# Performance work log

Measured on AMD Instinct MI355X. Metric: run time of the kernel, lower is better.

## Reference

```python
import jax, jax.numpy as jnp
import numpy as np

B, N, E = 64, 2048, 32768          # graphs, nodes/graph, edges/graph
DIM = 64
RATIO = 0.8
K1 = int(np.ceil(RATIO * N))        # 1639 nodes/graph after pool1
K2 = int(np.ceil(RATIO * K1))       # 1312 nodes/graph after pool2
NUM_CLASSES = 6


def gcn_conv(x, W, b, src, dst, valid, n):
    # GCNConv with self-loops: out = D^-1/2 (A+I) D^-1/2 (x W) + b
    xw = x @ W                                          # [n, DIM]
    deg = jnp.zeros(n, x.dtype).at[dst].add(valid) + 1.0  # in-degree incl. self-loop
    norm = valid * jax.lax.rsqrt(deg[src] * deg[dst])      # per-edge norm (0 for masked)
    agg = jnp.zeros_like(xw).at[dst].add(xw[src] * norm[:, None])
    return agg + xw / deg[:, None] + b                  # self-loop term has norm 1/deg


def topk_pool(x, p, n_graphs, n_per, k):
    # PyG TopKPooling: score = tanh(x.p/||p||); keep top-k per graph; gate x by score
    score = jnp.tanh((x @ p) / jnp.linalg.norm(p))       # [n_graphs*n_per]
    vals, idx = jax.lax.top_k(score.reshape(n_graphs, n_per), k)  # [n_graphs, k]
    xg = x.reshape(n_graphs, n_per, -1)
    sel = jnp.take_along_axis(xg, idx[..., None], axis=1)          # [n_graphs, k, DIM]
    xp = sel * vals[..., None]
    perm = (idx + (jnp.arange(n_graphs) * n_per)[:, None]).reshape(-1)  # global ids kept
    return xp.reshape(n_graphs * k, -1), perm


def global_max_mean(x, n_graphs, n_per):
    xg = x.reshape(n_graphs, n_per, -1)
    return jnp.concatenate([xg.max(axis=1), xg.mean(axis=1)], axis=1)  # [n_graphs, 2*DIM]


def forward(x, edge_index, batch, W1, b1, p1, W2, b2, p2, lin1_w, lin1_b, lin2_w, lin2_b):
    src, dst = edge_index[0], edge_index[1]
    n_total = B * N
    ones = jnp.ones(src.shape[0], x.dtype)

    x = jax.nn.relu(gcn_conv(x, W1, b1, src, dst, ones, n_total))
    x, perm = topk_pool(x, p1, B, N, K1)
    x1 = global_max_mean(x, B, K1)

    # filter_adj: reindex edges to surviving nodes; drop (mask) edges touching removed nodes
    new_id = jnp.full(n_total, -1, jnp.int32).at[perm].set(jnp.arange(B * K1, dtype=jnp.int32))
    s2, d2 = new_id[src], new_id[dst]
    valid = ((s2 >= 0) & (d2 >= 0)).astype(x.dtype)
    s2 = jnp.where(s2 >= 0, s2, 0)
    d2 = jnp.where(d2 >= 0, d2, 0)

    x = jax.nn.relu(gcn_conv(x, W2, b2, s2, d2, valid, B * K1))
    x, _ = topk_pool(x, p2, B, K1, K2)
    x2 = global_max_mean(x, B, K2)

    h = x1 + x2
    h = jax.nn.relu(h @ lin1_w + lin1_b)
    return h @ lin2_w + lin2_b                           # [B, NUM_CLASSES]


def setup_inputs():
    key = jax.random.key(0)
    ks = jax.random.split(key, 10)
    x = jax.random.normal(ks[0], (B * N, DIM), jnp.float32)
    off = (jnp.arange(B) * N)[:, None]
    src = (jax.random.randint(ks[1], (B, E), 0, N) + off).reshape(-1)
    dst = (jax.random.randint(ks[2], (B, E), 0, N) + off).reshape(-1)
    edge_index = jnp.stack([src, dst]).astype(jnp.int32)
    batch = jnp.repeat(jnp.arange(B, dtype=jnp.int32), N)
    s = 1.0 / np.sqrt(DIM)
    return {
        "x": x,
        "edge_index": edge_index,
        "batch": batch,
        "W1": jax.random.normal(ks[3], (DIM, DIM), jnp.float32) * s,
        "b1": jnp.zeros(DIM, jnp.float32),
        "p1": jax.random.normal(ks[4], (DIM,), jnp.float32) * s,
        "W2": jax.random.normal(ks[5], (DIM, DIM), jnp.float32) * s,
        "b2": jnp.zeros(DIM, jnp.float32),
        "p2": jax.random.normal(ks[6], (DIM,), jnp.float32) * s,
        "lin1_w": jax.random.normal(ks[7], (2 * DIM, DIM), jnp.float32) / np.sqrt(2 * DIM),
        "lin1_b": jnp.zeros(DIM, jnp.float32),
        "lin2_w": jax.random.normal(ks[8], (DIM, NUM_CLASSES), jnp.float32) * s,
        "lin2_b": jnp.zeros(NUM_CLASSES, jnp.float32),
    }


def reference(x, edge_index, batch, W1, b1, p1, W2, b2, p2, lin1_w, lin1_b, lin2_w, lin2_b):
    return forward(x, edge_index, batch, W1, b1, p1, W2, b2, p2, lin1_w, lin1_b, lin2_w, lin2_b)
```

## Files before the change

kernel.cpp:

```cpp
#include <hip/hip_runtime.h>
#include <hip/hip_bf16.h>
#include <cstdint>
#include <cstddef>

#define B_    64
#define N_    2048
#define E_    32768
#define DIM_  64
#define K1_   1639
#define K2_   1312
#define NTOT  (B_ * N_)
#define ETOT  (B_ * E_)
#define N2TOT (B_ * K1_)
#define NCLS  6
#define PB_   8
#define CHUNKS_ 16
#define SLICES_ 16
#define BCAP  3072
#define REG_  192

typedef short bf8 __attribute__((ext_vector_type(8)));
typedef float f4  __attribute__((ext_vector_type(4)));

static __device__ __forceinline__ float2 bf2f(unsigned u) {
    float2 r;
    r.x = __uint_as_float(u << 16);
    r.y = __uint_as_float(u & 0xFFFF0000u);
    return r;
}
static __device__ __forceinline__ unsigned f2bf(float a, float b) {
    __hip_bfloat162 h = __float22bfloat162_rn(make_float2(a, b));
    unsigned u;
    __builtin_memcpy(&u, &h, 4);
    return u;
}
static __device__ __forceinline__ unsigned short f2bf_rn(float v) {
    unsigned u = __float_as_uint(v);
    return (unsigned short)((u + 0x7FFFu + ((u >> 16) & 1u)) >> 16);
}
static __device__ __forceinline__ unsigned long long mk_key(float s, int i) {
    unsigned u = __float_as_uint(s);
    u = (u & 0x80000000u) ? ~u : (u | 0x80000000u);
    return ((unsigned long long)u << 11) | (unsigned long long)(2047 - i);
}

template<int STAGE>
__launch_bounds__(256)
__global__ void k_bucket(const int* src, const int* dst, const int* remap,
                         int* bcnt, unsigned int* blist) {
    const int LSTR = (STAGE == 1) ? 128 : 103;
    __shared__ unsigned int lb[CHUNKS_][REG_];
    __shared__ int lc[CHUNKS_];
    __shared__ int rm[N_];
    int b = blockIdx.x;
    int g = b & 63, slice = b >> 6;
    int tid = threadIdx.x;
    if (tid < CHUNKS_) lc[tid] = 0;
    if (STAGE == 2)
        for (int i = tid; i < N_; i += 256) rm[i] = remap[g * N_ + i];
    __syncthreads();
    const int ESL = E_ / SLICES_;
    const int* sp = src + (size_t)g * E_ + slice * ESL;
    const int* dp = dst + (size_t)g * E_ + slice * ESL;
    int gbase = g * ((STAGE == 1) ? N_ : K1_);
    for (int e = tid * 4; e < ESL; e += 1024) {
        int4 ss = *(const int4*)&sp[e];
        int4 dd = *(const int4*)&dp[e];
#pragma unroll
        for (int t = 0; t < 4; t++) {
            int s = (&ss.x)[t], d = (&dd.x)[t];
            if (STAGE == 2) {
                s = rm[s & (N_ - 1)]; d = rm[d & (N_ - 1)];
                if ((s | d) < 0) continue;
                s -= gbase; d -= gbase;
            } else {
                s &= (N_ - 1); d &= (N_ - 1);
            }
            int ch = d / LSTR;
            int dl = d - ch * LSTR;
            int p = atomicAdd(&lc[ch], 1);
            if (p < REG_) lb[ch][p] = ((unsigned)dl << 12) | (unsigned)s;
        }
    }
    __syncthreads();
    for (int ch = 0; ch < CHUNKS_; ch++) {
        int n = min(lc[ch], REG_);
        unsigned int* out = blist + (size_t)(g * CHUNKS_ + ch) * BCAP + slice * REG_;
        for (int i = tid; i < n; i += 256) out[i] = lb[ch][i];
    }
    if (tid < CHUNKS_) bcnt[(g * SLICES_ + slice) * CHUNKS_ + tid] = min(lc[tid], REG_);
}

template<int STAGE>
__launch_bounds__(256)
__global__ void k_sort(const int* bcnt, unsigned int* blist,
                       const float* xf, const unsigned int* xg,
                       unsigned int* xb, int* ninfo) {
    const int NL   = (STAGE == 1) ? N_ : K1_;
    const int LSTR = (STAGE == 1) ? 128 : 103;
    __shared__ int cnt[128], st[128], cur[128], cnt_s[SLICES_], stot[2];
    __shared__ float rsqv[128];
    __shared__ unsigned short sorted[BCAP];
    int b = blockIdx.x;
    int g = b & 63, ch = b >> 6;
    int tid = threadIdx.x;
    if (tid < 128) { cnt[tid] = 0; cur[tid] = 0; }
    if (tid < SLICES_) cnt_s[tid] = bcnt[(g * SLICES_ + tid) * CHUNKS_ + ch];
    __syncthreads();
    size_t bb = (size_t)(g * CHUNKS_ + ch) * BCAP;
    const unsigned int* bl = blist + bb;
    const int TOT = SLICES_ * REG_;
    for (int i = tid; i < TOT; i += 256) {
        int s = i / REG_, j = i - s * REG_;
        if (j < cnt_s[s]) atomicAdd(&cnt[bl[i] >> 12], 1);
    }
    __syncthreads();
    if (tid < 128) {
        int v = cnt[tid];
        int l64 = tid & 63;
#pragma unroll
        for (int o = 1; o < 64; o <<= 1) {
            int t = __shfl_up(v, o);
            if (l64 >= o) v += t;
        }
        st[tid] = v;
        if (l64 == 63) stot[tid >> 6] = v;
    }
    __syncthreads();
    if (tid >= 64 && tid < 128) st[tid] += stot[0];
    __syncthreads();
    for (int i = tid; i < TOT; i += 256) {
        int s = i / REG_, j = i - s * REG_;
        if (j < cnt_s[s]) {
            unsigned pk = bl[i];
            int dl = (int)(pk >> 12);
            int p = st[dl] - cnt[dl] + atomicAdd(&cur[dl], 1);
            sorted[p] = (unsigned short)(pk & 0xFFFu);
        }
    }
    __syncthreads();
    int n = st[127];
    for (int i = tid; i < n; i += 256) blist[bb + i] = ((unsigned int)sorted[i]) << 5;
    int lo = ch * LSTR;
    int nloc = min(LSTR, NL - lo);
    int gbase = g * NL;
    if (tid < nloc) {
        int node = gbase + lo + tid;
        int c = cnt[tid];
        int start = (int)bb + st[tid] - c;
        ninfo[node] = (start << 8) | min(c, 255);
        rsqv[tid] = rsqrtf((float)(c + 1));
    }
    __syncthreads();
    for (int idx = tid; idx < nloc * 32; idx += 256) {
        int nl = idx >> 5, f2 = idx & 31;
        int node = gbase + lo + nl;
        float sc = rsqv[nl];
        float2 v;
        if (STAGE == 1) v = ((const float2*)xf)[(size_t)node * 32 + f2];
        else            v = bf2f(xg[(size_t)node * 32 + f2]);
        xb[(size_t)node * 32 + f2] = f2bf(v.x * sc, v.y * sc);
    }
}

template<bool GATE>
__launch_bounds__(256)
__global__ void k_agg(const unsigned int* xb, const int* ninfo, const unsigned int* csr,
                      float* y) {
    int b = blockIdx.x;
    int xcd = b & 7, r = b >> 3;
    int wid = threadIdx.x >> 6, lane = threadIdx.x & 63;
    int half = lane >> 5;
    int sub = wid * 2 + half;
    int graph, local;
    if (GATE) {
        graph = xcd * 8 + r / 205;
        local = (r % 205) * 8 + sub;
        if (local >= K1_) return;
    } else {
        graph = xcd * 8 + (r >> 8);
        local = (r & 255) * 8 + sub;
    }
    const int NL = GATE ? K1_ : N_;
    int node = graph * NL + local;
    int l32 = lane & 31;
    int hbase = half << 5;
    int ni = ninfo[node];
    int cnt = ni & 255, base = ni >> 8;
    float rd = rsqrtf((float)(cnt + 1));
    float a0x = 0.f, a0y = 0.f, a1x = 0.f, a1y = 0.f;
    float a2x = 0.f, a2y = 0.f, a3x = 0.f, a3y = 0.f;
    int gbase32 = graph * NL * 32;
    for (int chunk = 0; chunk < cnt; chunk += 32) {
        int nch = min(32, cnt - chunk);
        int sv = 0;
        if (l32 < nch) sv = gbase32 + (int)csr[base + chunk + l32];
        int i = 0;
        for (; i + 4 <= nch; i += 4) {
            int e0 = __shfl(sv, hbase + i);
            int e1 = __shfl(sv, hbase + i + 1);
            int e2 = __shfl(sv, hbase + i + 2);
            int e3 = __shfl(sv, hbase + i + 3);
            unsigned u0 = xb[(size_t)(e0 + l32)];
            unsigned u1 = xb[(size_t)(e1 + l32)];
            unsigned u2 = xb[(size_t)(e2 + l32)];
            unsigned u3 = xb[(size_t)(e3 + l32)];
            float2 f0 = bf2f(u0), f1 = bf2f(u1), f2 = bf2f(u2), f3 = bf2f(u3);
            a0x += f0.x; a0y += f0.y;
            a1x += f1.x; a1y += f1.y;
            a2x += f2.x; a2y += f2.y;
            a3x += f3.x; a3y += f3.y;
        }
        for (; i < nch; i++) {
            int e0 = __shfl(sv, hbase + i);
            float2 f0 = bf2f(xb[(size_t)(e0 + l32)]);
            a0x += f0.x; a0y += f0.y;
        }
    }
    float sx = (a0x + a1x) + (a2x + a3x);
    float sy = (a0y + a1y) + (a2y + a3y);
    float2 fs = bf2f(xb[(size_t)node * 32 + l32]);
    float2 o;
    o.x = (sx + fs.x) * rd;
    o.y = (sy + fs.y) * rd;
    ((float2*)y)[(size_t)node * 32 + l32] = o;
}

__launch_bounds__(256)
__global__ void k_convrow(float* y, const float* W, const float* bias, const float* pvec,
                          float* score, int rows) {
    int wid  = threadIdx.x >> 6;
    int lane = threadIdx.x & 63;
    int rowbase = blockIdx.x * 64 + wid * 16;
    int q = lane >> 4, c = lane & 15;
    bf8 bh[2][4], blo[2][4];
#pragma unroll
    for (int ks = 0; ks < 2; ks++)
#pragma unroll
        for (int nt = 0; nt < 4; nt++) {
            bf8 h, l;
#pragma unroll
            for (int j = 0; j < 8; j++) {
                float wv = W[(ks * 32 + q * 8 + j) * 64 + nt * 16 + c];
                unsigned short hb = f2bf_rn(wv);
                h[j] = (short)hb;
                l[j] = (short)f2bf_rn(wv - __uint_as_float((unsigned)hb << 16));
            }
            bh[ks][nt] = h; blo[ks][nt] = l;
        }
    const float* yr = y + (size_t)(rowbase + c) * DIM_ + q * 8;
    bf8 ah[2], al[2];
#pragma unroll
    for (int ks = 0; ks < 2; ks++) {
        float4 v0 = *(const float4*)(yr + ks * 32);
        float4 v1 = *(const float4*)(yr + ks * 32 + 4);
        float vv[8] = {v0.x, v0.y, v0.z, v0.w, v1.x, v1.y, v1.z, v1.w};
        bf8 h, l;
#pragma unroll
        for (int j = 0; j < 8; j++) {
            unsigned short hb = f2bf_rn(vv[j]);
            h[j] = (short)hb;
            l[j] = (short)f2bf_rn(vv[j] - __uint_as_float((unsigned)hb << 16));
        }
        ah[ks] = h; al[ks] = l;
    }
    float pp = 0.f;
#pragma unroll
    for (int i = 0; i < DIM_; i++) pp += pvec[i] * pvec[i];
    float rpn = rsqrtf(pp);
    float dot[4] = {0.f, 0.f, 0.f, 0.f};
#pragma unroll
    for (int nt = 0; nt < 4; nt++) {
        f4 acc = {0.f, 0.f, 0.f, 0.f};
#pragma unroll
        for (int ks = 0; ks < 2; ks++) {
            acc = __builtin_amdgcn_mfma_f32_16x16x32_bf16(ah[ks], bh[ks][nt],  acc, 0, 0, 0);
            acc = __builtin_amdgcn_mfma_f32_16x16x32_bf16(ah[ks], blo[ks][nt], acc, 0, 0, 0);
            acc = __builtin_amdgcn_mfma_f32_16x16x32_bf16(al[ks], bh[ks][nt],  acc, 0, 0, 0);
        }
        float bcol = bias[nt * 16 + c];
        float pcol = pvec[nt * 16 + c];
        float st[4];
#pragma unroll
        for (int reg = 0; reg < 4; reg++) {
            float v = fmaxf(acc[reg] + bcol, 0.f);
            st[reg] = v;
            dot[reg] += v * pcol;
        }
#pragma unroll
        for (int reg = 0; reg < 4; reg++)
            y[(size_t)(rowbase + q * 4 + reg) * DIM_ + nt * 16 + c] = st[reg];
    }
#pragma unroll
    for (int m = 1; m < 16; m <<= 1) {
#pragma unroll
        for (int reg = 0; reg < 4; reg++) dot[reg] += __shfl_xor(dot[reg], m);
    }
    if (c == 0) {
#pragma unroll
        for (int reg = 0; reg < 4; reg++)
            score[rowbase + q * 4 + reg] = tanhf(dot[reg] * rpn);
    }
    (void)rows;
}

template<int STAGE>
__launch_bounds__(256)
__global__ void k_thresh(const float* score, unsigned long long* thresh) {
    const int Nin = (STAGE == 1) ? N_ : K1_;
    const int K   = (STAGE == 1) ? K1_ : K2_;
    __shared__ unsigned long long keys[N_];
    __shared__ int bins[256], wsum[4];
    __shared__ unsigned long long s_prefix;
    __shared__ int s_need;
    int g = blockIdx.x, tid = threadIdx.x;
    int l64 = tid & 63, wid = tid >> 6;
    const float* sg = score + (size_t)g * Nin;
    for (int i = tid; i < Nin; i += 256) keys[i] = mk_key(sg[i], i);
    if (tid == 0) { s_need = K; s_prefix = 0ull; }
    __syncthreads();
    for (int shift = 40; shift >= 0; shift -= 8) {
        bins[tid] = 0;
        __syncthreads();
        unsigned long long pref = s_prefix;
        int need = s_need;
        int hi = shift + 8;
        for (int i = tid; i < Nin; i += 256) {
            unsigned long long k = keys[i];
            if ((k >> hi) == pref) atomicAdd(&bins[(int)((k >> shift) & 255)], 1);
        }
        __syncthreads();
        int mine = bins[tid];
        int v = mine;
#pragma unroll
        for (int o = 1; o < 64; o <<= 1) {
            int t = __shfl_down(v, o);
            if (l64 + o < 64) v += t;
        }
        if (l64 == 0) wsum[wid] = v;
        __syncthreads();
        for (int w = wid + 1; w < 4; w++) v += wsum[w];
        int nxt = v - mine;
        if (v >= need && nxt < need) {
            s_prefix = (pref << 8) | (unsigned long long)tid;
            s_need = need - nxt;
        }
        __syncthreads();
    }
    if (tid == 0) thresh[g] = s_prefix;
}

template<int STAGE>
__launch_bounds__(256)
__global__ void k_pool(const float* score, const float* conv, const unsigned long long* thresh,
                       int* new_id, unsigned int* xg, float* part) {
    const int Nin = (STAGE == 1) ? N_ : K1_;
    const int RNG = (STAGE == 1) ? (N_ / PB_) : ((K1_ + PB_ - 1) / PB_);
    __shared__ int rnk[256];
    __shared__ unsigned char keepf[256];
    __shared__ int wsum[4], s_base[4];
    __shared__ float rmx[4][64], rsm[4][64];
    int b = blockIdx.x;
    int g = b & 63, pb = b >> 6;
    int tid = threadIdx.x;
    int l64 = tid & 63, wid = tid >> 6;
    const float* sg = score + (size_t)g * Nin;
    unsigned long long T = thresh[g];
    int R0 = pb * RNG;
    int R1 = min(R0 + RNG, Nin);
    if (STAGE == 1) {
        int cb = 0;
        for (int i = tid; i < R0; i += 256) cb += (mk_key(sg[i], i) >= T) ? 1 : 0;
#pragma unroll
        for (int o = 32; o; o >>= 1) cb += __shfl_down(cb, o);
        if (l64 == 0) s_base[wid] = cb;
        int i = R0 + tid;
        int keep = (i < R1 && mk_key(sg[i], i) >= T) ? 1 : 0;
        keepf[tid] = (unsigned char)keep;
        int v = keep;
#pragma unroll
        for (int o = 1; o < 64; o <<= 1) {
            int t = __shfl_up(v, o);
            if (l64 >= o) v += t;
        }
        if (l64 == 63) wsum[wid] = v;
        __syncthreads();
        int base = s_base[0] + s_base[1] + s_base[2] + s_base[3];
        int wbase = 0;
        for (int w = 0; w < wid; w++) wbase += wsum[w];
        int r = base + wbase + v - keep;
        rnk[tid] = r;
        if (i < Nin) new_id[g * N_ + i] = keep ? (g * K1_ + r) : -1;
    } else {
        int i = R0 + tid;
        keepf[tid] = (unsigned char)((i < R1 && mk_key(sg[i], i) >= T) ? 1 : 0);
    }
    __syncthreads();
    float mx = -3.402823466e38f, sm = 0.f;
    for (int i = R0 + wid; i < R1; i += 4) {
        if (!keepf[i - R0]) continue;
        float val = sg[i];
        float v = conv[(size_t)(g * Nin + i) * DIM_ + l64] * val;
        mx = fmaxf(mx, v);
        sm += v;
        if (STAGE == 1) {
            unsigned pk = f2bf(v, __shfl_xor(v, 1));
            if (!(l64 & 1)) xg[(size_t)(g * K1_ + rnk[i - R0]) * 32 + (l64 >> 1)] = pk;
        }
    }
    rmx[wid][l64] = mx; rsm[wid][l64] = sm;
    __syncthreads();
    if (wid == 0) {
        mx = fmaxf(fmaxf(rmx[0][l64], rmx[1][l64]), fmaxf(rmx[2][l64], rmx[3][l64]));
        sm = rsm[0][l64] + rsm[1][l64] + rsm[2][l64] + rsm[3][l64];
        part[((size_t)(g * PB_ + pb) * 2 + 0) * 64 + l64] = mx;
        part[((size_t)(g * PB_ + pb) * 2 + 1) * 64 + l64] = sm;
    }
}

__launch_bounds__(64)
__global__ void k_head(const float* part1, const float* part2,
                       const float* l1w, const float* l1b,
                       const float* l2w, const float* l2b, float* out) {
    __shared__ float h[128];
    __shared__ float h1[64];
    int g = blockIdx.x, t = threadIdx.x;
    float mx1 = -3.402823466e38f, sm1 = 0.f, mx2 = -3.402823466e38f, sm2 = 0.f;
#pragma unroll
    for (int c = 0; c < PB_; c++) {
        mx1 = fmaxf(mx1, part1[((size_t)(g * PB_ + c) * 2 + 0) * 64 + t]);
        sm1 += part1[((size_t)(g * PB_ + c) * 2 + 1) * 64 + t];
        mx2 = fmaxf(mx2, part2[((size_t)(g * PB_ + c) * 2 + 0) * 64 + t]);
        sm2 += part2[((size_t)(g * PB_ + c) * 2 + 1) * 64 + t];
    }
    h[t]      = mx1 + mx2;
    h[t + 64] = sm1 / (float)K1_ + sm2 / (float)K2_;
    __syncthreads();
    float acc = l1b[t];
#pragma unroll 8
    for (int i = 0; i < 128; i++) acc += h[i] * l1w[i * 64 + t];
    h1[t] = fmaxf(acc, 0.0f);
    __syncthreads();
    if (t < NCLS) {
        float o = l2b[t];
#pragma unroll
        for (int i = 0; i < 64; i++) o += h1[i] * l2w[i * NCLS + t];
        out[g * NCLS + t] = o;
    }
}

extern "C" void kernel_launch(void* const* d_in, const int* in_sizes, int n_in,
                              void* d_out, int out_size, void* d_ws, size_t ws_size,
                              hipStream_t stream) {
    const float* x   = (const float*)d_in[0];
    const int*   ei  = (const int*)d_in[1];
    const int*   src = ei;
    const int*   dst = ei + ETOT;
    const float* W1  = (const float*)d_in[3];
    const float* b1  = (const float*)d_in[4];
    const float* p1  = (const float*)d_in[5];
    const float* W2  = (const float*)d_in[6];
    const float* b2  = (const float*)d_in[7];
    const float* p2  = (const float*)d_in[8];
    const float* l1w = (const float*)d_in[9];
    const float* l1b = (const float*)d_in[10];
    const float* l2w = (const float*)d_in[11];
    const float* l2b = (const float*)d_in[12];
    (void)in_sizes; (void)n_in; (void)out_size; (void)ws_size;

    char* ws = (char*)d_ws;
    size_t off = 0;
    auto alloc = [&](size_t bytes) -> void* {
        void* p = ws + off;
        off = (off + bytes + 255) & ~(size_t)255;
        return p;
    };
    float*              bufA   = (float*)             alloc((size_t)NTOT  * DIM_ * 4);
    float*              bufB   = (float*)             alloc((size_t)N2TOT * DIM_ * 4);
    unsigned int*       blist  = (unsigned int*)      alloc((size_t)B_ * CHUNKS_ * BCAP * 4);
    unsigned int*       xb     = (unsigned int*)      alloc((size_t)NTOT * 32 * 4);
    int*                bcnt   = (int*)               alloc((size_t)B_ * SLICES_ * CHUNKS_ * 4);
    int*                ninfo  = (int*)               alloc((size_t)NTOT * 4);
    float*              score  = (float*)             alloc((size_t)NTOT * 4);
    int*                newid  = (int*)               alloc((size_t)NTOT * 4);
    unsigned long long* thr    = (unsigned long long*)alloc((size_t)B_ * 8);
    float*              part1  = (float*)             alloc((size_t)B_ * PB_ * 128 * 4);
    float*              part2  = (float*)             alloc((size_t)B_ * PB_ * 128 * 4);
    unsigned int*       xg     = (unsigned int*)bufB;

    k_bucket<1><<<B_ * SLICES_, 256, 0, stream>>>(src, dst, nullptr, bcnt, blist);
    k_sort<1><<<B_ * CHUNKS_, 256, 0, stream>>>(bcnt, blist, x, nullptr, xb, ninfo);
    k_agg<false><<<NTOT / 8, 256, 0, stream>>>(xb, ninfo, blist, bufA);
    k_convrow<<<NTOT / 64, 256, 0, stream>>>(bufA, W1, b1, p1, score, NTOT);
    k_thresh<1><<<B_, 256, 0, stream>>>(score, thr);
    k_pool<1><<<B_ * PB_, 256, 0, stream>>>(score, bufA, thr, newid, xg, part1);

    k_bucket<2><<<B_ * SLICES_, 256, 0, stream>>>(src, dst, newid, bcnt, blist);
    k_sort<2><<<B_ * CHUNKS_, 256, 0, stream>>>(bcnt, blist, nullptr, xg, xb, ninfo);
    k_agg<true><<<205 * B_, 256, 0, stream>>>(xb, ninfo, blist, bufB);
    k_convrow<<<N2TOT / 64, 256, 0, stream>>>(bufB, W2, b2, p2, score, N2TOT);
    k_thresh<2><<<B_, 256, 0, stream>>>(score, thr);
    k_pool<2><<<B_ * PB_, 256, 0, stream>>>(score, bufB, thr, nullptr, nullptr, part2);

    k_head<<<B_, 64, 0, stream>>>(part1, part2, l1w, l1b, l2w, l2b, (float*)d_out);
}
```

Before: 320.3 us.

## Fuse neighbor aggregation with GCN linear transform via LDS staging

Merges the gather-aggregate kernel and the MFMA row-transform kernel into one kernel per stage. Each block aggregates 64 rows into a swizzled LDS tile and feeds the MFMA transform straight from LDS, so the fp32 intermediate no longer round-trips through global memory and one launch per stage disappears. It also prefetches the next node's CSR indices and unrolls the gather loop by 8 for more loads in flight. In exchange, each block now runs far more sequential work (8 nodes per half-wave), which cuts the number of blocks and may hide gather latency less well.

```diff
diff --git a/kernel.cpp b/kernel.cpp
--- a/kernel.cpp
+++ b/kernel.cpp
@@ -165,73 +165,116 @@
 
 template<bool GATE>
 __launch_bounds__(256)
-__global__ void k_agg(const unsigned int* xb, const int* ninfo, const unsigned int* csr,
-                      float* y) {
+__global__ void k_aggconv(const unsigned int* xb, const int* ninfo, const unsigned int* csr,
+                          const float* W, const float* bias, const float* pvec,
+                          float* y, float* score) {
+    const int NL = GATE ? K1_ : N_;
+    __shared__ float4 ls4[1024];
+    float* ls = (float*)ls4;
     int b = blockIdx.x;
-    int xcd = b & 7, r = b >> 3;
+    int wg;
+    if (GATE) {
+        int xcd = b & 7, k = b >> 3;
+        wg = (xcd < 7 ? xcd * 205 : 1435 + (xcd - 7) * 204) + k;
+    } else {
+        wg = (b & 7) * 256 + (b >> 3);
+    }
     int wid = threadIdx.x >> 6, lane = threadIdx.x & 63;
     int half = lane >> 5;
-    int sub = wid * 2 + half;
-    int graph, local;
-    if (GATE) {
-        graph = xcd * 8 + r / 205;
-        local = (r % 205) * 8 + sub;
-        if (local >= K1_) return;
-    } else {
-        graph = xcd * 8 + (r >> 8);
-        local = (r & 255) * 8 + sub;
-    }
-    const int NL = GATE ? K1_ : N_;
-    int node = graph * NL + local;
     int l32 = lane & 31;
     int hbase = half << 5;
-    int ni = ninfo[node];
-    int cnt = ni & 255, base = ni >> 8;
-    float rd = rsqrtf((float)(cnt + 1));
-    float a0x = 0.f, a0y = 0.f, a1x = 0.f, a1y = 0.f;
-    float a2x = 0.f, a2y = 0.f, a3x = 0.f, a3y = 0.f;
-    int gbase32 = graph * NL * 32;
-    for (int chunk = 0; chunk < cnt; chunk += 32) {
-        int nch = min(32, cnt - chunk);
-        int sv = 0;
-        if (l32 < nch) sv = gbase32 + (int)csr[base + chunk + l32];
-        int i = 0;
-        for (; i + 4 <= nch; i += 4) {
-            int e0 = __shfl(sv, hbase + i);
-            int e1 = __shfl(sv, hbase + i + 1);
-            int e2 = __shfl(sv, hbase + i + 2);
-            int e3 = __shfl(sv, hbase + i + 3);
-            unsigned u0 = xb[(size_t)(e0 + l32)];
-            unsigned u1 = xb[(size_t)(e1 + l32)];
-            unsigned u2 = xb[(size_t)(e2 + l32)];
-            unsigned u3 = xb[(size_t)(e3 + l32)];
-            float2 f0 = bf2f(u0), f1 = bf2f(u1), f2 = bf2f(u2), f3 = bf2f(u3);
-            a0x += f0.x; a0y += f0.y;
-            a1x += f1.x; a1y += f1.y;
-            a2x += f2.x; a2y += f2.y;
-            a3x += f3.x; a3y += f3.y;
-        }
-        for (; i < nch; i++) {
-            int e0 = __shfl(sv, hbase + i);
-            float2 f0 = bf2f(xb[(size_t)(e0 + l32)]);
-            a0x += f0.x; a0y += f0.y;
-        }
-    }
-    float sx = (a0x + a1x) + (a2x + a3x);
-    float sy = (a0y + a1y) + (a2y + a3y);
-    float2 fs = bf2f(xb[(size_t)node * 32 + l32]);
-    float2 o;
-    o.x = (sx + fs.x) * rd;
-    o.y = (sy + fs.y) * rd;
-    ((float2*)y)[(size_t)node * 32 + l32] = o;
-}
-
-__launch_bounds__(256)
-__global__ void k_convrow(float* y, const float* W, const float* bias, const float* pvec,
-                          float* score, int rows) {
-    int wid  = threadIdx.x >> 6;
-    int lane = threadIdx.x & 63;
-    int rowbase = blockIdx.x * 64 + wid * 16;
+    int rowbase = wg * 64 + wid * 16;
+
+    int niv = 0;
+    if (lane < 16) niv = ninfo[rowbase + lane];
+    int ni = __shfl(niv, half);
+    int sv = 0;
+    {
+        int c0 = ni & 255;
+        if (l32 < c0) sv = (int)csr[(ni >> 8) + l32];
+    }
+#pragma unroll 1
+    for (int p = 0; p < 8; p++) {
+        int cnt = ni & 255, base = ni >> 8;
+        int ni_n = 0, sv_n = 0;
+        if (p < 7) {
+            ni_n = __shfl(niv, 2 * (p + 1) + half);
+            int cn = ni_n & 255;
+            if (l32 < cn) sv_n = (int)csr[(ni_n >> 8) + l32];
+        }
+        int rloc = wid * 16 + 2 * p + half;
+        int node = wg * 64 + rloc;
+        int gbase32 = GATE ? (node / K1_) * (K1_ * 32) : ((node & ~(N_ - 1)) * 32);
+        unsigned selfu = xb[(size_t)node * 32 + l32];
+        float a0x = 0.f, a0y = 0.f, a1x = 0.f, a1y = 0.f;
+        float a2x = 0.f, a2y = 0.f, a3x = 0.f, a3y = 0.f;
+        int svc = sv;
+        for (int chunk = 0; chunk < cnt; chunk += 32) {
+            int nch = min(32, cnt - chunk);
+            if (chunk) svc = (l32 < nch) ? (int)csr[base + chunk + l32] : 0;
+            int i = 0;
+            for (; i + 8 <= nch; i += 8) {
+                int e0 = __shfl(svc, hbase + i);
+                int e1 = __shfl(svc, hbase + i + 1);
+                int e2 = __shfl(svc, hbase + i + 2);
+                int e3 = __shfl(svc, hbase + i + 3);
+                int e4 = __shfl(svc, hbase + i + 4);
+                int e5 = __shfl(svc, hbase + i + 5);
+                int e6 = __shfl(svc, hbase + i + 6);
+                int e7 = __shfl(svc, hbase + i + 7);
+                unsigned u0 = xb[(size_t)(gbase32 + e0 + l32)];
+                unsigned u1 = xb[(size_t)(gbase32 + e1 + l32)];
+                unsigned u2 = xb[(size_t)(gbase32 + e2 + l32)];
+                unsigned u3 = xb[(size_t)(gbase32 + e3 + l32)];
+                unsigned u4 = xb[(size_t)(gbase32 + e4 + l32)];
+                unsigned u5 = xb[(size_t)(gbase32 + e5 + l32)];
+                unsigned u6 = xb[(size_t)(gbase32 + e6 + l32)];
+                unsigned u7 = xb[(size_t)(gbase32 + e7 + l32)];
+                float2 f0 = bf2f(u0), f1 = bf2f(u1), f2 = bf2f(u2), f3 = bf2f(u3);
+                float2 f4 = bf2f(u4), f5 = bf2f(u5), f6 = bf2f(u6), f7 = bf2f(u7);
+                a0x += f0.x; a0y += f0.y;
+                a1x += f1.x; a1y += f1.y;
+                a2x += f2.x; a2y += f2.y;
+                a3x += f3.x; a3y += f3.y;
+                a0x += f4.x; a0y += f4.y;
+                a1x += f5.x; a1y += f5.y;
+                a2x += f6.x; a2y += f6.y;
+                a3x += f7.x; a3y += f7.y;
+            }
+            for (; i + 4 <= nch; i += 4) {
+                int e0 = __shfl(svc, hbase + i);
+                int e1 = __shfl(svc, hbase + i + 1);
+                int e2 = __shfl(svc, hbase + i + 2);
+                int e3 = __shfl(svc, hbase + i + 3);
+                unsigned u0 = xb[(size_t)(gbase32 + e0 + l32)];
+                unsigned u1 = xb[(size_t)(gbase32 + e1 + l32)];
+                unsigned u2 = xb[(size_t)(gbase32 + e2 + l32)];
+                unsigned u3 = xb[(size_t)(gbase32 + e3 + l32)];
+                float2 f0 = bf2f(u0), f1 = bf2f(u1), f2 = bf2f(u2), f3 = bf2f(u3);
+                a0x += f0.x; a0y += f0.y;
+                a1x += f1.x; a1y += f1.y;
+                a2x += f2.x; a2y += f2.y;
+                a3x += f3.x; a3y += f3.y;
+            }
+            for (; i < nch; i++) {
+                int e0 = __shfl(svc, hbase + i);
+                float2 f0 = bf2f(xb[(size_t)(gbase32 + e0 + l32)]);
+                a0x += f0.x; a0y += f0.y;
+            }
+        }
+        float rd = rsqrtf((float)(cnt + 1));
+        float sx = (a0x + a1x) + (a2x + a3x);
+        float sy = (a0y + a1y) + (a2y + a3y);
+        float2 fs = bf2f(selfu);
+        float2 o;
+        o.x = (sx + fs.x) * rd;
+        o.y = (sy + fs.y) * rd;
+        int pi = rloc * 32 + ((((l32 >> 1) ^ (rloc & 7)) << 1) | (l32 & 1));
+        ((float2*)ls)[pi] = o;
+        ni = ni_n; sv = sv_n;
+    }
+    __syncthreads();
+
     int q = lane >> 4, c = lane & 15;
     bf8 bh[2][4], blo[2][4];
 #pragma unroll
@@ -248,12 +291,13 @@
             }
             bh[ks][nt] = h; blo[ks][nt] = l;
         }
-    const float* yr = y + (size_t)(rowbase + c) * DIM_ + q * 8;
+    int rl16 = (wid * 16 + c) * 16;
+    int cx = c & 7;
     bf8 ah[2], al[2];
 #pragma unroll
     for (int ks = 0; ks < 2; ks++) {
-        float4 v0 = *(const float4*)(yr + ks * 32);
-        float4 v1 = *(const float4*)(yr + ks * 32 + 4);
+        float4 v0 = ls4[rl16 + ((ks * 8 + q * 2 + 0) ^ cx)];
+        float4 v1 = ls4[rl16 + ((ks * 8 + q * 2 + 1) ^ cx)];
         float vv[8] = {v0.x, v0.y, v0.z, v0.w, v1.x, v1.y, v1.z, v1.w};
         bf8 h, l;
 #pragma unroll
@@ -289,7 +333,7 @@
         }
 #pragma unroll
         for (int reg = 0; reg < 4; reg++)
-            y[(size_t)(rowbase + q * 4 + reg) * DIM_ + nt * 16 + c] = st[reg];
+            y[(size_t)(wg * 64 + wid * 16 + q * 4 + reg) * DIM_ + nt * 16 + c] = st[reg];
     }
 #pragma unroll
     for (int m = 1; m < 16; m <<= 1) {
@@ -299,9 +343,8 @@
     if (c == 0) {
 #pragma unroll
         for (int reg = 0; reg < 4; reg++)
-            score[rowbase + q * 4 + reg] = tanhf(dot[reg] * rpn);
-    }
-    (void)rows;
+            score[wg * 64 + wid * 16 + q * 4 + reg] = tanhf(dot[reg] * rpn);
+    }
 }
 
 template<int STAGE>
@@ -490,15 +533,13 @@
 
     k_bucket<1><<<B_ * SLICES_, 256, 0, stream>>>(src, dst, nullptr, bcnt, blist);
     k_sort<1><<<B_ * CHUNKS_, 256, 0, stream>>>(bcnt, blist, x, nullptr, xb, ninfo);
-    k_agg<false><<<NTOT / 8, 256, 0, stream>>>(xb, ninfo, blist, bufA);
-    k_convrow<<<NTOT / 64, 256, 0, stream>>>(bufA, W1, b1, p1, score, NTOT);
+    k_aggconv<false><<<NTOT / 64, 256, 0, stream>>>(xb, ninfo, blist, W1, b1, p1, bufA, score);
     k_thresh<1><<<B_, 256, 0, stream>>>(score, thr);
     k_pool<1><<<B_ * PB_, 256, 0, stream>>>(score, bufA, thr, newid, xg, part1);
 
     k_bucket<2><<<B_ * SLICES_, 256, 0, stream>>>(src, dst, newid, bcnt, blist);
     k_sort<2><<<B_ * CHUNKS_, 256, 0, stream>>>(bcnt, blist, nullptr, xg, xb, ninfo);
-    k_agg<true><<<205 * B_, 256, 0, stream>>>(xb, ninfo, blist, bufB);
-    k_convrow<<<N2TOT / 64, 256, 0, stream>>>(bufB, W2, b2, p2, score, N2TOT);
+    k_aggconv<true><<<N2TOT / 64, 256, 0, stream>>>(xb, ninfo, blist, W2, b2, p2, bufB, score);
     k_thresh<2><<<B_, 256, 0, stream>>>(score, thr);
     k_pool<2><<<B_ * PB_, 256, 0, stream>>>(score, bufB, thr, nullptr, nullptr, part2);
 
```

Result: no change. 321.0 us (+0.2%).
